# Optimization experiments

Measured on AMD Instinct MI355X. Metric: run time of the kernel, lower is better.

Reference implementation:

```python
import jax, jax.numpy as jnp
import numpy as np
from jax import lax

B, NBB, C, H, W = 32, 16, 1024, 22, 22
P = 3            # pooled output size (3x3)
SCALE = 1.0 / 16.0
EPS = 1e-5


def setup_inputs() -> dict:
    key = jax.random.key(0)
    ks = jax.random.split(key, 12)
    feat = jax.random.normal(ks[0], (B, C, H, W), jnp.float32)
    # bbox in xywh image coords, in-range for a 352x352 search region
    xy = jax.random.uniform(ks[1], (B, NBB, 2), jnp.float32, 0.0, 250.0)
    wh = jax.random.uniform(ks[2], (B, NBB, 2), jnp.float32, 16.0, 100.0)
    bbox = jnp.concatenate([xy, wh], axis=-1)
    conv_w = jax.random.normal(ks[3], (C, C, 3, 3), jnp.float32) * 0.01
    conv_b = jnp.zeros((C,), jnp.float32)
    bn_gamma = jnp.ones((C,), jnp.float32)
    bn_beta = jnp.zeros((C,), jnp.float32)
    bn_mean = jax.random.normal(ks[4], (C,), jnp.float32) * 0.1
    bn_var = jax.random.uniform(ks[5], (C,), jnp.float32, 0.5, 1.5)
    w1 = jax.random.normal(ks[6], (C // 2, C), jnp.float32) * 0.02
    b1 = jnp.zeros((C // 2,), jnp.float32)
    w2 = jax.random.normal(ks[7], (C // 2, C // 2), jnp.float32) * 0.02
    b2 = jnp.zeros((C // 2,), jnp.float32)
    w3 = jax.random.normal(ks[8], (512, C // 2), jnp.float32) * 0.02
    b3 = jnp.zeros((512,), jnp.float32)
    return dict(feat=feat, bbox=bbox, conv_w=conv_w, conv_b=conv_b,
                bn_gamma=bn_gamma, bn_beta=bn_beta, bn_mean=bn_mean, bn_var=bn_var,
                w1=w1, b1=b1, w2=w2, b2=b2, w3=w3, b3=b3)


def _hat_int(t):
    # Antiderivative of the bilinear hat h(u)=max(0,1-|u|), clipped to support.
    t = jnp.clip(t, -1.0, 1.0)
    return t + 0.5 - 0.5 * t * jnp.abs(t)


def _bin_weights(lo, bw, n):
    # lo, bw: [B, NBB].  Returns exact integral weights [B, NBB, P, n]:
    # W[b,r,p,i] = integral over bin p of hat(x - i) dx  (PrRoI closed form).
    p = jnp.arange(P, dtype=lo.dtype)
    xs = lo[..., None] + p * bw[..., None]          # [B,NBB,P] bin starts
    xe = xs + bw[..., None]                          # bin ends
    i = jnp.arange(n, dtype=lo.dtype)
    return _hat_int(xe[..., None] - i) - _hat_int(xs[..., None] - i)


def reference(feat, bbox, conv_w, conv_b, bn_gamma, bn_beta, bn_mean, bn_var,
              w1, b1, w2, b2, w3, b3):
    # --- PrRoI pooling (exact separable bilinear integral) ---
    x1 = bbox[..., 0] * SCALE
    y1 = bbox[..., 1] * SCALE
    x2 = (bbox[..., 0] + bbox[..., 2]) * SCALE
    y2 = (bbox[..., 1] + bbox[..., 3]) * SCALE
    bw = (x2 - x1) / P
    bh = (y2 - y1) / P
    Wx = _bin_weights(x1, bw, W)                     # [B,NBB,P,W]
    Wy = _bin_weights(y1, bh, H)                     # [B,NBB,P,H]
    pooled = jnp.einsum('bchw,bnqh,bnpw->bncqp', feat, Wy, Wx)  # [B,NBB,C,P,P]
    area = jnp.maximum(bw * bh, 0.0)[..., None, None, None]
    pooled = jnp.where(area > 0, pooled / jnp.maximum(area, 1e-12), 0.0)
    x = pooled.reshape(B * NBB, C, P, P)

    # --- conv_bn_relu: 3x3 conv, valid padding -> 1x1, BN (eval), ReLU ---
    x = lax.conv_general_dilated(x, conv_w, (1, 1), 'VALID',
                                 dimension_numbers=('NCHW', 'OIHW', 'NCHW'))
    x = x + conv_b[:, None, None]
    x = (x - bn_mean[:, None, None]) * (bn_gamma * lax.rsqrt(bn_var + EPS))[:, None, None]
    x = x + bn_beta[:, None, None]
    x = jax.nn.relu(x)

    # --- MLP head ---
    x = x.reshape(B * NBB, C)
    x = jax.nn.relu(x @ w1.T + b1)
    x = jax.nn.relu(x @ w2.T + b2)
    x = x @ w3.T + b3
    return x.reshape(B, NBB, 512)
```

## Files before the change

kernel.cpp:

```cpp
#include <hip/hip_runtime.h>
#include <hip/hip_bf16.h>

#define B_    32
#define NBB_  16
#define C_    1024
#define H_    22
#define W_    22
#define NROI  512
#define KCONV 9216
#define SCALE_ (1.0f/16.0f)
#define EPS_  1e-5f

using f32x4  = __attribute__((ext_vector_type(4))) float;
using bf16x8 = __attribute__((ext_vector_type(8))) short;

__device__ __forceinline__ unsigned short f2bf(float f) {
  union { float f; unsigned u; } x; x.f = f;
  unsigned r = x.u + 0x7fffu + ((x.u >> 16) & 1u);
  return (unsigned short)(r >> 16);
}

__device__ __forceinline__ float hat_int(float t) {
  t = fminf(fmaxf(t, -1.f), 1.f);
  return t + 0.5f - 0.5f * t * fabsf(t);
}

__global__ __launch_bounds__(32) void prep_rois(const float* __restrict__ bbox,
                                                float* __restrict__ wy,
                                                float* __restrict__ wx) {
  int r = blockIdx.x;
  float4 bb = ((const float4*)bbox)[r];
  float x1 = bb.x * SCALE_, y1 = bb.y * SCALE_;
  float x2 = (bb.x + bb.z) * SCALE_, y2 = (bb.y + bb.w) * SCALE_;
  float bw = (x2 - x1) / 3.f, bh = (y2 - y1) / 3.f;
  float area = fmaxf(bw * bh, 0.f);
  float inv = area > 0.f ? 1.f / fmaxf(area, 1e-12f) : 0.f;
  int i = threadIdx.x;
  if (i < 22) {
    float fi = (float)i;
#pragma unroll
    for (int q = 0; q < 3; ++q) {
      float sy = y1 + q * bh;
      wy[r*66 + q*22 + i] = hat_int(sy + bh - fi) - hat_int(sy - fi);
      float sx = x1 + q * bw;
      wx[r*66 + q*22 + i] = (hat_int(sx + bw - fi) - hat_int(sx - fi)) * inv;
    }
  }
}

__global__ __launch_bounds__(256) void cvt_bf16(const float* __restrict__ src,
                                                unsigned short* __restrict__ dst, int n8) {
  int i = blockIdx.x * 256 + threadIdx.x;
  if (i >= n8) return;
  float4 a = ((const float4*)src)[2*i];
  float4 b = ((const float4*)src)[2*i + 1];
  uint4 pk;
  pk.x = (unsigned)f2bf(a.x) | ((unsigned)f2bf(a.y) << 16);
  pk.y = (unsigned)f2bf(a.z) | ((unsigned)f2bf(a.w) << 16);
  pk.z = (unsigned)f2bf(b.x) | ((unsigned)f2bf(b.y) << 16);
  pk.w = (unsigned)f2bf(b.z) | ((unsigned)f2bf(b.w) << 16);
  ((uint4*)dst)[i] = pk;
}

__global__ __launch_bounds__(256) void pool_kernel(const float* __restrict__ feat,
                                                   const float* __restrict__ wyg,
                                                   const float* __restrict__ wxg,
                                                   unsigned short* __restrict__ X) {
  __shared__ __align__(16) float featS[16 * 484];
  __shared__ float wyS[NBB_ * 66];
  __shared__ float wxS[NBB_ * 66];
  int tid = threadIdx.x;
  int cb = blockIdx.x;
  int b  = blockIdx.y;
  const float4* f4 = (const float4*)(feat + ((size_t)b * C_ + (size_t)cb * 16) * 484);
#pragma unroll
  for (int i = 0; i < 8; ++i) {
    int idx = tid + i * 256;
    if (idx < 1936) ((float4*)featS)[idx] = f4[idx];
  }
  const float* wysrc = wyg + (size_t)b * NBB_ * 66;
  const float* wxsrc = wxg + (size_t)b * NBB_ * 66;
  for (int idx = tid; idx < NBB_ * 66; idx += 256) { wyS[idx] = wysrc[idx]; wxS[idx] = wxsrc[idx]; }
  __syncthreads();

  int cl = tid & 15, n = tid >> 4;
  const float* fp = featS + cl * 484;
  float wxr[3][22];
#pragma unroll
  for (int p = 0; p < 3; ++p)
#pragma unroll
    for (int w = 0; w < 22; ++w) wxr[p][w] = wxS[n*66 + p*22 + w];

  float out[3][3] = {};
  for (int h = 0; h < 22; ++h) {
    float wy0 = wyS[n*66 + h], wy1 = wyS[n*66 + 22 + h], wy2 = wyS[n*66 + 44 + h];
    float cs0 = 0.f, cs1 = 0.f, cs2 = 0.f;
#pragma unroll
    for (int w = 0; w < 22; ++w) {
      float f = fp[h*22 + w];
      cs0 += f * wxr[0][w];
      cs1 += f * wxr[1][w];
      cs2 += f * wxr[2][w];
    }
    out[0][0] += wy0*cs0; out[0][1] += wy0*cs1; out[0][2] += wy0*cs2;
    out[1][0] += wy1*cs0; out[1][1] += wy1*cs1; out[1][2] += wy1*cs2;
    out[2][0] += wy2*cs0; out[2][1] += wy2*cs1; out[2][2] += wy2*cs2;
  }
  unsigned short* xp = X + (size_t)(b*NBB_ + n) * KCONV + (size_t)(cb*16 + cl) * 9;
#pragma unroll
  for (int q = 0; q < 3; ++q)
#pragma unroll
    for (int p = 0; p < 3; ++p) xp[q*3 + p] = f2bf(out[q][p]);
}

__global__ __launch_bounds__(256) void gemm_nt(const unsigned short* __restrict__ A,
                                               const unsigned short* __restrict__ Bm,
                                               float* __restrict__ Cp,
                                               int M, int N, int K, int kChunk) {
  __shared__ __align__(16) unsigned short As[64][40];
  __shared__ __align__(16) unsigned short Bs[64][40];
  int tid = threadIdx.x;
  int lane = tid & 63, wid = tid >> 6;
  int wm = wid >> 1, wn = wid & 1;
  int l15 = lane & 15, kg = lane >> 4;
  int nt = blockIdx.x, mt = blockIdx.y, z = blockIdx.z;
  int kbeg = z * kChunk;
  int kend = kbeg + kChunk; if (kend > K) kend = K;
  int srow = tid >> 2, sseg = tid & 3;
  const unsigned short* aG = A  + (size_t)(mt*64 + srow) * K + sseg * 8;
  const unsigned short* bG = Bm + (size_t)(nt*64 + srow) * K + sseg * 8;
  f32x4 acc[2][2] = {};

  for (int k0 = kbeg; k0 < kend; k0 += 32) {
    uint4 av = *(const uint4*)(aG + k0);
    uint4 bv = *(const uint4*)(bG + k0);
    __syncthreads();
    *(uint4*)&As[srow][sseg*8] = av;
    *(uint4*)&Bs[srow][sseg*8] = bv;
    __syncthreads();
    bf16x8 a0 = *(const bf16x8*)&As[wm*32 +      l15][kg*8];
    bf16x8 a1 = *(const bf16x8*)&As[wm*32 + 16 + l15][kg*8];
    bf16x8 b0 = *(const bf16x8*)&Bs[wn*32 +      l15][kg*8];
    bf16x8 b1 = *(const bf16x8*)&Bs[wn*32 + 16 + l15][kg*8];
    acc[0][0] = __builtin_amdgcn_mfma_f32_16x16x32_bf16(a0, b0, acc[0][0], 0, 0, 0);
    acc[0][1] = __builtin_amdgcn_mfma_f32_16x16x32_bf16(a0, b1, acc[0][1], 0, 0, 0);
    acc[1][0] = __builtin_amdgcn_mfma_f32_16x16x32_bf16(a1, b0, acc[1][0], 0, 0, 0);
    acc[1][1] = __builtin_amdgcn_mfma_f32_16x16x32_bf16(a1, b1, acc[1][1], 0, 0, 0);
  }

  float* cp = Cp + ((size_t)z * M + (size_t)mt * 64) * N + (size_t)nt * 64;
#pragma unroll
  for (int fm = 0; fm < 2; ++fm)
#pragma unroll
    for (int fn = 0; fn < 2; ++fn)
#pragma unroll
      for (int r = 0; r < 4; ++r) {
        int row = wm*32 + fm*16 + kg*4 + r;
        int col = wn*32 + fn*16 + l15;
        cp[(size_t)row * N + col] = acc[fm][fn][r];
      }
}

template<int MODE>
__global__ __launch_bounds__(256) void epi(const float* __restrict__ Cp, int SK, int MN4, int N,
                                           const float* __restrict__ bias,
                                           const float* __restrict__ g,
                                           const float* __restrict__ be,
                                           const float* __restrict__ mu,
                                           const float* __restrict__ var,
                                           unsigned short* __restrict__ outb,
                                           float* __restrict__ outf) {
  int i = blockIdx.x * 256 + threadIdx.x;
  if (i >= MN4) return;
  float4 s = ((const float4*)Cp)[i];
  for (int z = 1; z < SK; ++z) {
    float4 t = ((const float4*)Cp)[(size_t)z * MN4 + i];
    s.x += t.x; s.y += t.y; s.z += t.z; s.w += t.w;
  }
  int n0 = (i * 4) % N;
  float v[4] = {s.x, s.y, s.z, s.w};
  if (MODE == 0) {
    unsigned short o[4];
#pragma unroll
    for (int j = 0; j < 4; ++j) {
      int n = n0 + j;
      float sc = g[n] * rsqrtf(var[n] + EPS_);
      float t = (v[j] + bias[n] - mu[n]) * sc + be[n];
      o[j] = f2bf(fmaxf(t, 0.f));
    }
    uint2 pk; pk.x = (unsigned)o[0] | ((unsigned)o[1] << 16);
    pk.y = (unsigned)o[2] | ((unsigned)o[3] << 16);
    *(uint2*)&outb[(size_t)i * 4] = pk;
  } else if (MODE == 1) {
    unsigned short o[4];
#pragma unroll
    for (int j = 0; j < 4; ++j) o[j] = f2bf(fmaxf(v[j] + bias[n0 + j], 0.f));
    uint2 pk; pk.x = (unsigned)o[0] | ((unsigned)o[1] << 16);
    pk.y = (unsigned)o[2] | ((unsigned)o[3] << 16);
    *(uint2*)&outb[(size_t)i * 4] = pk;
  } else {
    float4 o;
    o.x = v[0] + bias[n0];     o.y = v[1] + bias[n0 + 1];
    o.z = v[2] + bias[n0 + 2]; o.w = v[3] + bias[n0 + 3];
    ((float4*)outf)[i] = o;
  }
}

extern "C" void kernel_launch(void* const* d_in, const int* in_sizes, int n_in,
                              void* d_out, int out_size, void* d_ws, size_t ws_size,
                              hipStream_t stream) {
  const float* feat   = (const float*)d_in[0];
  const float* bbox   = (const float*)d_in[1];
  const float* conv_w = (const float*)d_in[2];
  const float* conv_b = (const float*)d_in[3];
  const float* gamma  = (const float*)d_in[4];
  const float* beta   = (const float*)d_in[5];
  const float* mean   = (const float*)d_in[6];
  const float* var    = (const float*)d_in[7];
  const float* w1     = (const float*)d_in[8];
  const float* b1     = (const float*)d_in[9];
  const float* w2     = (const float*)d_in[10];
  const float* b2     = (const float*)d_in[11];
  const float* w3     = (const float*)d_in[12];
  const float* b3     = (const float*)d_in[13];

  char* ws = (char*)d_ws;
  float*          wy  = (float*)(ws);
  float*          wx  = (float*)(ws + 135168);
  unsigned short* Xb  = (unsigned short*)(ws + 270336);
  unsigned short* Wfb = (unsigned short*)(ws + 9707520);
  unsigned short* w1b = (unsigned short*)(ws + 28581888);
  unsigned short* w2b = (unsigned short*)(ws + 29630464);
  unsigned short* w3b = (unsigned short*)(ws + 30154752);
  float*          part= (float*)(ws + 30679040);
  unsigned short* H0  = (unsigned short*)(ws + 39067648);
  unsigned short* H1  = (unsigned short*)(ws + 40116224);
  unsigned short* H2  = (unsigned short*)(ws + 40640512);

  prep_rois<<<NROI, 32, 0, stream>>>(bbox, wy, wx);
  cvt_bf16<<<(1179648 + 255) / 256, 256, 0, stream>>>(conv_w, Wfb, 1179648);
  cvt_bf16<<<(65536 + 255) / 256, 256, 0, stream>>>(w1, w1b, 65536);
  cvt_bf16<<<(32768 + 255) / 256, 256, 0, stream>>>(w2, w2b, 32768);
  cvt_bf16<<<(32768 + 255) / 256, 256, 0, stream>>>(w3, w3b, 32768);
  pool_kernel<<<dim3(64, 32), 256, 0, stream>>>(feat, wy, wx, Xb);

  gemm_nt<<<dim3(16, 8, 4), 256, 0, stream>>>(Xb, Wfb, part, 512, 1024, 9216, 2304);
  epi<0><<<(131072 + 255) / 256, 256, 0, stream>>>(part, 4, 131072, 1024,
      conv_b, gamma, beta, mean, var, H0, nullptr);

  gemm_nt<<<dim3(8, 8, 4), 256, 0, stream>>>(H0, w1b, part, 512, 512, 1024, 256);
  epi<1><<<(65536 + 255) / 256, 256, 0, stream>>>(part, 4, 65536, 512,
      b1, nullptr, nullptr, nullptr, nullptr, H1, nullptr);

  gemm_nt<<<dim3(8, 8, 4), 256, 0, stream>>>(H1, w2b, part, 512, 512, 512, 128);
  epi<1><<<(65536 + 255) / 256, 256, 0, stream>>>(part, 4, 65536, 512,
      b2, nullptr, nullptr, nullptr, nullptr, H2, nullptr);

  gemm_nt<<<dim3(8, 8, 4), 256, 0, stream>>>(H2, w3b, part, 512, 512, 512, 128);
  epi<2><<<(65536 + 255) / 256, 256, 0, stream>>>(part, 4, 65536, 512,
      b3, nullptr, nullptr, nullptr, nullptr, nullptr, (float*)d_out);
}
```

Before: 128.6 us.

## Use MFMA for PrRoI pooling and a 128-tile async-LDS GEMM for the conv

Rewrites the pooling kernel so the W-direction contraction runs as bf16 MFMA over feature rows staged in LDS, with the H-direction weights applied as scalar FMAs on the MFMA outputs. Replaces the conv GEMM with a 128x128 tile kernel that uses global_load_lds double buffering and an XOR-swizzled LDS layout, and doubles the split-K factor to 8. The intent is to cut the scalar FMA cost of pooling and improve data reuse and load/compute overlap in the large GEMM. In exchange, pooling now rounds features and weights to bf16 before contraction, and the larger split-K partial buffer forces H0-H2 to move in the workspace.

```diff
diff --git a/kernel.cpp b/kernel.cpp
--- a/kernel.cpp
+++ b/kernel.cpp
@@ -23,6 +23,11 @@
 __device__ __forceinline__ float hat_int(float t) {
   t = fminf(fmaxf(t, -1.f), 1.f);
   return t + 0.5f - 0.5f * t * fabsf(t);
+}
+
+__device__ __forceinline__ void glds16(const void* g, void* l) {
+  __builtin_amdgcn_global_load_lds((const __attribute__((address_space(1))) void*)g,
+                                   (__attribute__((address_space(3))) void*)l, 16, 0, 0);
 }
 
 __global__ __launch_bounds__(32) void prep_rois(const float* __restrict__ bbox,
@@ -62,55 +67,153 @@
   ((uint4*)dst)[i] = pk;
 }
 
-__global__ __launch_bounds__(256) void pool_kernel(const float* __restrict__ feat,
-                                                   const float* __restrict__ wyg,
-                                                   const float* __restrict__ wxg,
-                                                   unsigned short* __restrict__ X) {
-  __shared__ __align__(16) float featS[16 * 484];
-  __shared__ float wyS[NBB_ * 66];
-  __shared__ float wxS[NBB_ * 66];
+__global__ __launch_bounds__(192) void pool_mfma(const float* __restrict__ feat,
+                                                 const float* __restrict__ wyg,
+                                                 const float* __restrict__ wxg,
+                                                 unsigned short* __restrict__ X) {
+  __shared__ __align__(16) unsigned short A[22*16*40];
+  __shared__ __align__(16) unsigned short Bx[48*32];
+  __shared__ float wyS[16*66];
   int tid = threadIdx.x;
-  int cb = blockIdx.x;
-  int b  = blockIdx.y;
+  int cb = blockIdx.x, b = blockIdx.y;
+
   const float4* f4 = (const float4*)(feat + ((size_t)b * C_ + (size_t)cb * 16) * 484);
-#pragma unroll
-  for (int i = 0; i < 8; ++i) {
-    int idx = tid + i * 256;
-    if (idx < 1936) ((float4*)featS)[idx] = f4[idx];
-  }
-  const float* wysrc = wyg + (size_t)b * NBB_ * 66;
-  const float* wxsrc = wxg + (size_t)b * NBB_ * 66;
-  for (int idx = tid; idx < NBB_ * 66; idx += 256) { wyS[idx] = wysrc[idx]; wxS[idx] = wxsrc[idx]; }
+  for (int i = tid; i < 1936; i += 192) {
+    float4 v = f4[i];
+    int lin = i * 4;
+    {
+      int c = lin / 484, rem = lin - c * 484, h = rem / 22, w = rem - h * 22;
+      unsigned pk = (unsigned)f2bf(v.x) | ((unsigned)f2bf(v.y) << 16);
+      *(unsigned*)&A[(h*16 + c)*40 + w] = pk;
+    }
+    {
+      int lin2 = lin + 2;
+      int c = lin2 / 484, rem = lin2 - c * 484, h = rem / 22, w = rem - h * 22;
+      unsigned pk = (unsigned)f2bf(v.z) | ((unsigned)f2bf(v.w) << 16);
+      *(unsigned*)&A[(h*16 + c)*40 + w] = pk;
+    }
+  }
+  for (int z = tid; z < 352*5; z += 192) {
+    int row = z / 5, j = z - row * 5;
+    *(unsigned*)&A[row*40 + 22 + j*2] = 0u;
+  }
+  if (tid < 48) {
+    int n = tid / 3, p = tid - n * 3;
+    const float* wxp = wxg + ((size_t)b * 16 + n) * 66 + p * 22;
+#pragma unroll
+    for (int w = 0; w < 22; w += 2) {
+      unsigned pk = (unsigned)f2bf(wxp[w]) | ((unsigned)f2bf(wxp[w+1]) << 16);
+      *(unsigned*)&Bx[tid*32 + w] = pk;
+    }
+#pragma unroll
+    for (int w = 22; w < 32; w += 2) *(unsigned*)&Bx[tid*32 + w] = 0u;
+  }
+  for (int i = tid; i < 1056; i += 192) wyS[i] = wyg[(size_t)b * 1056 + i];
   __syncthreads();
 
-  int cl = tid & 15, n = tid >> 4;
-  const float* fp = featS + cl * 484;
-  float wxr[3][22];
-#pragma unroll
-  for (int p = 0; p < 3; ++p)
-#pragma unroll
-    for (int w = 0; w < 22; ++w) wxr[p][w] = wxS[n*66 + p*22 + w];
-
-  float out[3][3] = {};
-  for (int h = 0; h < 22; ++h) {
-    float wy0 = wyS[n*66 + h], wy1 = wyS[n*66 + 22 + h], wy2 = wyS[n*66 + 44 + h];
-    float cs0 = 0.f, cs1 = 0.f, cs2 = 0.f;
-#pragma unroll
-    for (int w = 0; w < 22; ++w) {
-      float f = fp[h*22 + w];
-      cs0 += f * wxr[0][w];
-      cs1 += f * wxr[1][w];
-      cs2 += f * wxr[2][w];
-    }
-    out[0][0] += wy0*cs0; out[0][1] += wy0*cs1; out[0][2] += wy0*cs2;
-    out[1][0] += wy1*cs0; out[1][1] += wy1*cs1; out[1][2] += wy1*cs2;
-    out[2][0] += wy2*cs0; out[2][1] += wy2*cs1; out[2][2] += wy2*cs2;
-  }
-  unsigned short* xp = X + (size_t)(b*NBB_ + n) * KCONV + (size_t)(cb*16 + cl) * 9;
-#pragma unroll
-  for (int q = 0; q < 3; ++q)
-#pragma unroll
-    for (int p = 0; p < 3; ++p) xp[q*3 + p] = f2bf(out[q][p]);
+  int lane = tid & 63, wid = tid >> 6;
+  int l15 = lane & 15, kg = lane >> 4;
+  int np = wid * 16 + l15;
+  int n = np / 3, p = np - n * 3;
+  bf16x8 bfrag = *(const bf16x8*)&Bx[np*32 + kg*8];
+  const float* wyp = wyS + n * 66;
+  const unsigned short* Abase = A + l15*40 + kg*8;
+
+  f32x4 zero = {};
+  f32x4 acc0 = {}, acc1 = {}, acc2 = {};
+  bf16x8 a0 = *(const bf16x8*)&Abase[0];
+  f32x4 t0 = __builtin_amdgcn_mfma_f32_16x16x32_bf16(a0, bfrag, zero, 0, 0, 0);
+#pragma unroll
+  for (int h = 0; h < 21; ++h) {
+    bf16x8 a1 = *(const bf16x8*)&Abase[(h+1)*640];
+    f32x4 t1 = __builtin_amdgcn_mfma_f32_16x16x32_bf16(a1, bfrag, zero, 0, 0, 0);
+    acc0 += t0 * wyp[h];
+    acc1 += t0 * wyp[22 + h];
+    acc2 += t0 * wyp[44 + h];
+    t0 = t1;
+  }
+  acc0 += t0 * wyp[21];
+  acc1 += t0 * wyp[43];
+  acc2 += t0 * wyp[65];
+
+  unsigned short* xrow = X + ((size_t)b*16 + n) * KCONV + (size_t)cb * 144;
+#pragma unroll
+  for (int r = 0; r < 4; ++r) {
+    int base = (kg*4 + r) * 9 + p;
+    xrow[base]     = f2bf(acc0[r]);
+    xrow[base + 3] = f2bf(acc1[r]);
+    xrow[base + 6] = f2bf(acc2[r]);
+  }
+}
+
+__global__ __launch_bounds__(256) void gemm128(const unsigned short* __restrict__ A,
+                                               const unsigned short* __restrict__ Bm,
+                                               float* __restrict__ Cp,
+                                               int M, int N, int K, int kChunk) {
+  __shared__ __align__(16) unsigned short As[2][4096];
+  __shared__ __align__(16) unsigned short Bs[2][4096];
+  int tid = threadIdx.x;
+  int lane = tid & 63, wid = tid >> 6;
+  int wm = wid >> 1, wn = wid & 1;
+  int l15 = lane & 15, kg = lane >> 4;
+  int nt = blockIdx.x, mt = blockIdx.y, z = blockIdx.z;
+  int kbeg = z * kChunk;
+  int steps = kChunk / 32;
+
+  int row0 = tid >> 2, row1 = 64 + row0;
+  int slot = tid & 3;
+  int s0 = slot ^ ((row0 >> 1) & 3);
+  int s1 = slot ^ ((row1 >> 1) & 3);
+  const unsigned short* ga0 = A  + (size_t)(mt*128 + row0) * K + kbeg + s0*8;
+  const unsigned short* ga1 = A  + (size_t)(mt*128 + row1) * K + kbeg + s1*8;
+  const unsigned short* gb0 = Bm + (size_t)(nt*128 + row0) * K + kbeg + s0*8;
+  const unsigned short* gb1 = Bm + (size_t)(nt*128 + row1) * K + kbeg + s1*8;
+  int wbyte = wid * 1024;
+
+  f32x4 acc[4][4] = {};
+  int cur = 0;
+
+#define ISSUE(buf, s) do { int ko = (s) * 32; \
+    glds16(ga0 + ko, (char*)&As[(buf)][0] + wbyte); \
+    glds16(ga1 + ko, (char*)&As[(buf)][0] + 4096 + wbyte); \
+    glds16(gb0 + ko, (char*)&Bs[(buf)][0] + wbyte); \
+    glds16(gb1 + ko, (char*)&Bs[(buf)][0] + 4096 + wbyte); } while (0)
+
+  ISSUE(0, 0);
+  for (int s = 0; s < steps; ++s) {
+    __syncthreads();
+    if (s + 1 < steps) ISSUE(cur ^ 1, s + 1);
+    bf16x8 af[4], bfr[4];
+#pragma unroll
+    for (int fm = 0; fm < 4; ++fm) {
+      int fr = wm*64 + fm*16 + l15;
+      af[fm] = *(const bf16x8*)&As[cur][fr*32 + ((kg ^ ((fr >> 1) & 3)) << 3)];
+    }
+#pragma unroll
+    for (int fn = 0; fn < 4; ++fn) {
+      int fr = wn*64 + fn*16 + l15;
+      bfr[fn] = *(const bf16x8*)&Bs[cur][fr*32 + ((kg ^ ((fr >> 1) & 3)) << 3)];
+    }
+#pragma unroll
+    for (int fm = 0; fm < 4; ++fm)
+#pragma unroll
+      for (int fn = 0; fn < 4; ++fn)
+        acc[fm][fn] = __builtin_amdgcn_mfma_f32_16x16x32_bf16(af[fm], bfr[fn], acc[fm][fn], 0, 0, 0);
+    cur ^= 1;
+  }
+#undef ISSUE
+
+  float* cp = Cp + ((size_t)z * M + (size_t)mt * 128) * N + (size_t)nt * 128;
+#pragma unroll
+  for (int fm = 0; fm < 4; ++fm)
+#pragma unroll
+    for (int fn = 0; fn < 4; ++fn)
+#pragma unroll
+      for (int r = 0; r < 4; ++r) {
+        int row = wm*64 + fm*16 + kg*4 + r;
+        int col = wn*64 + fn*16 + l15;
+        cp[(size_t)row * N + col] = acc[fm][fn][r];
+      }
 }
 
 __global__ __launch_bounds__(256) void gemm_nt(const unsigned short* __restrict__ A,
@@ -233,19 +336,19 @@
   unsigned short* w2b = (unsigned short*)(ws + 29630464);
   unsigned short* w3b = (unsigned short*)(ws + 30154752);
   float*          part= (float*)(ws + 30679040);
-  unsigned short* H0  = (unsigned short*)(ws + 39067648);
-  unsigned short* H1  = (unsigned short*)(ws + 40116224);
-  unsigned short* H2  = (unsigned short*)(ws + 40640512);
+  unsigned short* H0  = (unsigned short*)(ws + 47456256);
+  unsigned short* H1  = (unsigned short*)(ws + 48504832);
+  unsigned short* H2  = (unsigned short*)(ws + 49029120);
 
   prep_rois<<<NROI, 32, 0, stream>>>(bbox, wy, wx);
   cvt_bf16<<<(1179648 + 255) / 256, 256, 0, stream>>>(conv_w, Wfb, 1179648);
   cvt_bf16<<<(65536 + 255) / 256, 256, 0, stream>>>(w1, w1b, 65536);
   cvt_bf16<<<(32768 + 255) / 256, 256, 0, stream>>>(w2, w2b, 32768);
   cvt_bf16<<<(32768 + 255) / 256, 256, 0, stream>>>(w3, w3b, 32768);
-  pool_kernel<<<dim3(64, 32), 256, 0, stream>>>(feat, wy, wx, Xb);
-
-  gemm_nt<<<dim3(16, 8, 4), 256, 0, stream>>>(Xb, Wfb, part, 512, 1024, 9216, 2304);
-  epi<0><<<(131072 + 255) / 256, 256, 0, stream>>>(part, 4, 131072, 1024,
+  pool_mfma<<<dim3(64, 32), 192, 0, stream>>>(feat, wy, wx, Xb);
+
+  gemm128<<<dim3(8, 4, 8), 256, 0, stream>>>(Xb, Wfb, part, 512, 1024, 9216, 1152);
+  epi<0><<<(131072 + 255) / 256, 256, 0, stream>>>(part, 8, 131072, 1024,
       conv_b, gamma, beta, mean, var, H0, nullptr);
 
   gemm_nt<<<dim3(8, 8, 4), 256, 0, stream>>>(H0, w1b, part, 512, 512, 1024, 256);
```

Result: faster. 117.5 us (-8.6%).
